# Optimization experiments

Hardware: AMD Instinct MI355X
Metric: run time of the kernel (lower is better)

Reference implementation:

```python
import jax, jax.numpy as jnp
import numpy as np

MARGIN = 50.0

def setup_inputs() -> dict:
    key = jax.random.key(0)
    k1, k2 = jax.random.split(key)
    N, D = 4096, 768
    rep_anchor = jax.random.normal(k1, (N, D), dtype=jnp.float32)
    rep_pos = jax.random.normal(k2, (N, D), dtype=jnp.float32)
    return {"rep_anchor": rep_anchor, "rep_pos": rep_pos}

def reference(rep_anchor, rep_pos):
    # pairwise euclidean distances: dist[i, j] = ||anchor_i - pos_j||_2
    # (F.pairwise_distance with p=2, eps handled implicitly; use stable sqrt)
    a2 = jnp.sum(rep_anchor * rep_anchor, axis=1, keepdims=True)   # [N,1]
    p2 = jnp.sum(rep_pos * rep_pos, axis=1, keepdims=True).T       # [1,N]
    cross = rep_anchor @ rep_pos.T                                  # [N,N]
    sq = jnp.maximum(a2 + p2 - 2.0 * cross, 0.0)
    dist = jnp.sqrt(sq + 1e-12)
    scores = MARGIN - dist                                          # [N,N]
    # row-wise negative log-softmax, take diagonal (positive pair at index i)
    logp = jax.nn.log_softmax(scores, axis=1)
    loss_per_row = -jnp.diagonal(logp)                               # [N]
    return loss_per_row.mean()
```

## Files before the change

kernel.cpp:

```cpp
#include <hip/hip_runtime.h>
#include <hip/hip_bf16.h>
#include <hip/hip_fp8.h>
#include <stdint.h>


#define N_ROWS 4096
#define D_DIM  768
#define GRID_DIM (N_ROWS / 128)
#define NITER (D_DIM / 64)

typedef float f32x4 __attribute__((ext_vector_type(4)));
typedef int   i32x4 __attribute__((ext_vector_type(4)));

__global__ __launch_bounds__(256) void cvt_norms(
        const float* __restrict__ A, const float* __restrict__ P,
        uint8_t* __restrict__ A8, uint8_t* __restrict__ P8,
        float* __restrict__ a2, float* __restrict__ p2, float* __restrict__ S) {
    const int t = threadIdx.x, lane = t & 63, wave = t >> 6;
    const int row = blockIdx.x * 4 + wave;
    const float* src = blockIdx.y ? P : A;
    uint8_t* dst = blockIdx.y ? P8 : A8;
    float* nrm = blockIdx.y ? p2 : a2;

    const float4* s4 = (const float4*)src + (size_t)row * (D_DIM / 4);
    uint32_t* d4 = (uint32_t*)dst + (size_t)row * (D_DIM / 4);
    float s = 0.0f;
#pragma unroll
    for (int c = 0; c < 3; c++) {
        const int wf = c * 64 + lane;
        float4 v = s4[wf];
        s += v.x * v.x + v.y * v.y + v.z * v.z + v.w * v.w;
        union { uint32_t u; uint8_t b[4]; } pk;
        pk.b[0] = __hip_fp8_e4m3(v.x).__x;
        pk.b[1] = __hip_fp8_e4m3(v.y).__x;
        pk.b[2] = __hip_fp8_e4m3(v.z).__x;
        pk.b[3] = __hip_fp8_e4m3(v.w).__x;
        const int kb = wf >> 4, w16 = wf & 15;
        const int gw = w16 >> 1, h = w16 & 1;
        const int gp = ((gw & 3) << 1) | (gw >> 2);
        d4[(kb << 4) + (gp << 1) + h] = pk.u;
    }
    for (int off = 32; off; off >>= 1) s += __shfl_down(s, off);
    if (lane == 0) {
        nrm[row] = s;
        if (blockIdx.y == 0) S[row] = 0.0f;
    }
}

__device__ __forceinline__ void g2l16(const void* g, void* l) {
    __builtin_amdgcn_global_load_lds(
        (const __attribute__((address_space(1))) void*)g,
        (__attribute__((address_space(3))) void*)l, 16, 0, 0);
}

__global__ __launch_bounds__(256) void gemm_fused(
        const uint8_t* __restrict__ A8, const uint8_t* __restrict__ P8,
        const float* __restrict__ a2, const float* __restrict__ p2,
        float* __restrict__ S, float* __restrict__ Dd) {
    __shared__ __align__(16) uint8_t As[2][128 * 64];
    __shared__ __align__(16) uint8_t Bs[2][128 * 64];

    const int bm = blockIdx.x, bn = blockIdx.y;
    const int t = threadIdx.x;
    const int lane = t & 63, wave = t >> 6;
    const int wm = wave >> 1, wn = wave & 1;

    f32x4 acc[4][4];
#pragma unroll
    for (int i = 0; i < 4; i++)
#pragma unroll
        for (int j = 0; j < 4; j++) acc[i][j] = (f32x4){0.f, 0.f, 0.f, 0.f};

    const int gT = ((t & 3) - (t >> 3)) & 3;
    const size_t aBase = (size_t)(bm * 128 + (t >> 2)) * D_DIM + (size_t)gT * 16;
    const size_t bBase = (size_t)(bn * 128 + (t >> 2)) * D_DIM + (size_t)gT * 16;

    const int fr = lane & 15, fq = lane >> 4;
    int aOff[4], bOff[4];
#pragma unroll
    for (int mi = 0; mi < 4; mi++) {
        const int R = wm * 64 + mi * 16 + fr;
        aOff[mi] = R * 64 + ((fq + (R >> 1)) & 3) * 16;
    }
#pragma unroll
    for (int ni = 0; ni < 4; ni++) {
        const int R = wn * 64 + ni * 16 + fr;
        bOff[ni] = R * 64 + ((fq + (R >> 1)) & 3) * 16;
    }

#define STAGE(K2, SEL)                                                            \
    do {                                                                          \
        const int k0_ = (K2) * 64;                                                \
        _Pragma("unroll")                                                         \
        for (int c = 0; c < 2; c++)                                               \
            g2l16(A8 + aBase + (size_t)c * (64 * D_DIM) + k0_,                    \
                  &As[SEL][(c * 256 + t) * 16]);                                  \
        _Pragma("unroll")                                                         \
        for (int c = 0; c < 2; c++)                                               \
            g2l16(P8 + bBase + (size_t)c * (64 * D_DIM) + k0_,                    \
                  &Bs[SEL][(c * 256 + t) * 16]);                                  \
    } while (0)

    STAGE(0, 0);

    for (int k = 0; k < NITER; k++) {
        const int cur = k & 1;
        asm volatile("s_waitcnt vmcnt(0)" ::: "memory");
        asm volatile("s_barrier" ::: "memory");
        if (k + 1 < NITER) STAGE(k + 1, cur ^ 1);

        i32x4 av[4], bv[4];
#pragma unroll
        for (int mi = 0; mi < 4; mi++)
            av[mi] = *(const i32x4*)&As[cur][aOff[mi]];
#pragma unroll
        for (int ni = 0; ni < 4; ni++)
            bv[ni] = *(const i32x4*)&Bs[cur][bOff[ni]];
#pragma unroll
        for (int step = 0; step < 2; step++) {
#pragma unroll
            for (int mi = 0; mi < 4; mi++) {
                const long long afh = ((const long long*)&av[mi])[step];
#pragma unroll
                for (int ni = 0; ni < 4; ni++) {
                    const long long bfh = ((const long long*)&bv[ni])[step];
                    acc[mi][ni] = __builtin_amdgcn_mfma_f32_16x16x32_fp8_fp8(
                        afh, bfh, acc[mi][ni], 0, 0, 0);
                }
            }
        }
    }
#undef STAGE

    float p2v[4];
#pragma unroll
    for (int ni = 0; ni < 4; ni++)
        p2v[ni] = p2[bn * 128 + wn * 64 + ni * 16 + fr];
    const int colBase = bn * 128 + wn * 64 + fr;

#pragma unroll
    for (int mi = 0; mi < 4; mi++) {
#pragma unroll
        for (int r = 0; r < 4; r++) {
            const int gi = bm * 128 + wm * 64 + mi * 16 + fq * 4 + r;
            const float a2v = a2[gi];
            float rs = 0.0f;
#pragma unroll
            for (int ni = 0; ni < 4; ni++) {
                const float cross = acc[mi][ni][r];
                const float sq = a2v + p2v[ni] - 2.0f * cross;
                const float dist = sqrtf(fmaxf(sq, 0.0f) + 1e-12f);
                const int gj = colBase + ni * 16;
                if (gi == gj) Dd[gi] = dist;
                rs += __expf(-dist);
            }
            rs += __shfl_xor(rs, 1);
            rs += __shfl_xor(rs, 2);
            rs += __shfl_xor(rs, 4);
            rs += __shfl_xor(rs, 8);
            if (fr == 0) atomicAdd(&S[gi], rs);
        }
    }
}

__global__ void finalize(const float* __restrict__ S, const float* __restrict__ Dd,
                         float* __restrict__ out) {
    const int t = threadIdx.x;
    float s = 0.0f;
    for (int i = t; i < N_ROWS; i += 256) s += Dd[i] + logf(S[i]);
    for (int off = 32; off; off >>= 1) s += __shfl_down(s, off);
    __shared__ float wsum[4];
    if ((t & 63) == 0) wsum[t >> 6] = s;
    __syncthreads();
    if (t == 0) out[0] = (wsum[0] + wsum[1] + wsum[2] + wsum[3]) * (1.0f / N_ROWS);
}

__global__ void zero_out1(float* __restrict__ out) {
    if (threadIdx.x == 0 && blockIdx.x == 0) out[0] = 0.0f;
}
__global__ void naive_row(const float* __restrict__ A, const float* __restrict__ P,
                          float* __restrict__ out) {
    __shared__ float arow[D_DIM];
    const int i = blockIdx.x, t = threadIdx.x;
    for (int c = t; c < D_DIM; c += 256) arow[c] = A[(size_t)i * D_DIM + c];
    __syncthreads();
    float sumexp = 0.0f, ddiag = 0.0f;
    for (int j = t; j < N_ROWS; j += 256) {
        const float* p = P + (size_t)j * D_DIM;
        float d2 = 0.0f;
        for (int c = 0; c < D_DIM; c++) { float df = arow[c] - p[c]; d2 += df * df; }
        float dist = sqrtf(fmaxf(d2, 0.0f) + 1e-12f);
        if (j == i) ddiag = dist;
        sumexp += __expf(-dist);
    }
    for (int off = 32; off; off >>= 1) {
        sumexp += __shfl_down(sumexp, off);
        ddiag  += __shfl_down(ddiag, off);
    }
    __shared__ float w1[4], w2[4];
    if ((t & 63) == 0) { w1[t >> 6] = sumexp; w2[t >> 6] = ddiag; }
    __syncthreads();
    if (t == 0) {
        float se = w1[0] + w1[1] + w1[2] + w1[3];
        float dd = w2[0] + w2[1] + w2[2] + w2[3];
        atomicAdd(out, (dd + logf(se)) * (1.0f / N_ROWS));
    }
}

extern "C" void kernel_launch(void* const* d_in, const int* in_sizes, int n_in,
                              void* d_out, int out_size, void* d_ws, size_t ws_size,
                              hipStream_t stream) {
    const float* A = (const float*)d_in[0];
    const float* P = (const float*)d_in[1];
    float* out = (float*)d_out;

    const size_t F8_BYTES = (size_t)N_ROWS * D_DIM;
    const size_t V_BYTES  = (size_t)N_ROWS * sizeof(float);
    const size_t NEED = 2 * F8_BYTES + 4 * V_BYTES;

    if (ws_size >= NEED) {
        char* ws = (char*)d_ws;
        uint8_t* A8 = (uint8_t*)(ws);
        uint8_t* P8 = (uint8_t*)(ws + F8_BYTES);
        float* a2 = (float*)(ws + 2 * F8_BYTES);
        float* p2 = (float*)(ws + 2 * F8_BYTES + V_BYTES);
        float* S  = (float*)(ws + 2 * F8_BYTES + 2 * V_BYTES);
        float* Dd = (float*)(ws + 2 * F8_BYTES + 3 * V_BYTES);

        hipLaunchKernelGGL(cvt_norms, dim3(N_ROWS / 4, 2), dim3(256), 0, stream,
                           A, P, A8, P8, a2, p2, S);
        hipLaunchKernelGGL(gemm_fused, dim3(GRID_DIM, GRID_DIM), dim3(256), 0, stream,
                           A8, P8, a2, p2, S, Dd);
        hipLaunchKernelGGL(finalize, dim3(1), dim3(256), 0, stream, S, Dd, out);
    } else {
        hipLaunchKernelGGL(zero_out1, dim3(1), dim3(64), 0, stream, out);
        hipLaunchKernelGGL(naive_row, dim3(N_ROWS), dim3(256), 0, stream, A, P, out);
    }
}
```

Measured before the change: 114.7 us.

## Give each wave private LDS tiles to drop block barriers in FP8 GEMM

Each wave now loads its own 64-row A and B slices into a private LDS region, so the block-wide s_barrier in the K loop is removed and waves synchronise only through their own vmcnt waits. The pipeline is deepened to prefetch two stages ahead, waiting with vmcnt(8) instead of draining all loads each iteration. The cost is duplicated global-to-LDS traffic (the A and B tiles are loaded twice across waves) and LDS use rising from 32KB to 64KB per block, which may limit occupancy.

```diff
diff --git a/kernel.cpp b/kernel.cpp
--- a/kernel.cpp
+++ b/kernel.cpp
@@ -57,13 +57,13 @@
         const uint8_t* __restrict__ A8, const uint8_t* __restrict__ P8,
         const float* __restrict__ a2, const float* __restrict__ p2,
         float* __restrict__ S, float* __restrict__ Dd) {
-    __shared__ __align__(16) uint8_t As[2][128 * 64];
-    __shared__ __align__(16) uint8_t Bs[2][128 * 64];
+    __shared__ __align__(16) uint8_t L[4 * 2 * 8192];
 
     const int bm = blockIdx.x, bn = blockIdx.y;
     const int t = threadIdx.x;
     const int lane = t & 63, wave = t >> 6;
     const int wm = wave >> 1, wn = wave & 1;
+    const int wbase = wave * 16384;
 
     f32x4 acc[4][4];
 #pragma unroll
@@ -71,51 +71,55 @@
 #pragma unroll
         for (int j = 0; j < 4; j++) acc[i][j] = (f32x4){0.f, 0.f, 0.f, 0.f};
 
-    const int gT = ((t & 3) - (t >> 3)) & 3;
-    const size_t aBase = (size_t)(bm * 128 + (t >> 2)) * D_DIM + (size_t)gT * 16;
-    const size_t bBase = (size_t)(bn * 128 + (t >> 2)) * D_DIM + (size_t)gT * 16;
+    const int gT = ((lane & 3) - (lane >> 3)) & 3;
+    const size_t aBase = (size_t)(bm * 128 + wm * 64 + (lane >> 2)) * D_DIM + (size_t)gT * 16;
+    const size_t bBase = (size_t)(bn * 128 + wn * 64 + (lane >> 2)) * D_DIM + (size_t)gT * 16;
 
     const int fr = lane & 15, fq = lane >> 4;
     int aOff[4], bOff[4];
 #pragma unroll
     for (int mi = 0; mi < 4; mi++) {
-        const int R = wm * 64 + mi * 16 + fr;
+        const int R = mi * 16 + fr;
         aOff[mi] = R * 64 + ((fq + (R >> 1)) & 3) * 16;
     }
 #pragma unroll
     for (int ni = 0; ni < 4; ni++) {
-        const int R = wn * 64 + ni * 16 + fr;
+        const int R = ni * 16 + fr;
         bOff[ni] = R * 64 + ((fq + (R >> 1)) & 3) * 16;
     }
 
 #define STAGE(K2, SEL)                                                            \
     do {                                                                          \
         const int k0_ = (K2) * 64;                                                \
+        uint8_t* la_ = &L[wbase + (SEL) * 8192];                                  \
         _Pragma("unroll")                                                         \
-        for (int c = 0; c < 2; c++)                                               \
-            g2l16(A8 + aBase + (size_t)c * (64 * D_DIM) + k0_,                    \
-                  &As[SEL][(c * 256 + t) * 16]);                                  \
+        for (int c = 0; c < 4; c++)                                               \
+            g2l16(A8 + aBase + (size_t)c * (16 * D_DIM) + k0_,                    \
+                  la_ + c * 1024 + lane * 16);                                    \
         _Pragma("unroll")                                                         \
-        for (int c = 0; c < 2; c++)                                               \
-            g2l16(P8 + bBase + (size_t)c * (64 * D_DIM) + k0_,                    \
-                  &Bs[SEL][(c * 256 + t) * 16]);                                  \
+        for (int c = 0; c < 4; c++)                                               \
+            g2l16(P8 + bBase + (size_t)c * (16 * D_DIM) + k0_,                    \
+                  la_ + 4096 + c * 1024 + lane * 16);                             \
     } while (0)
 
     STAGE(0, 0);
+    STAGE(1, 1);
 
     for (int k = 0; k < NITER; k++) {
-        const int cur = k & 1;
-        asm volatile("s_waitcnt vmcnt(0)" ::: "memory");
-        asm volatile("s_barrier" ::: "memory");
-        if (k + 1 < NITER) STAGE(k + 1, cur ^ 1);
+        const int lb = wbase + (k & 1) * 8192;
+        if (k >= NITER - 1) asm volatile("s_waitcnt vmcnt(0)" ::: "memory");
+        else                asm volatile("s_waitcnt vmcnt(8)" ::: "memory");
 
         i32x4 av[4], bv[4];
 #pragma unroll
         for (int mi = 0; mi < 4; mi++)
-            av[mi] = *(const i32x4*)&As[cur][aOff[mi]];
+            av[mi] = *(const i32x4*)&L[lb + aOff[mi]];
 #pragma unroll
         for (int ni = 0; ni < 4; ni++)
-            bv[ni] = *(const i32x4*)&Bs[cur][bOff[ni]];
+            bv[ni] = *(const i32x4*)&L[lb + 4096 + bOff[ni]];
+        asm volatile("s_waitcnt lgkmcnt(0)" ::: "memory");
+        if (k + 2 < NITER) STAGE(k + 2, k & 1);
+
 #pragma unroll
         for (int step = 0; step < 2; step++) {
 #pragma unroll
```

After: 117.3 us. 1.02x slower.
